# Performance work log

Measured on AMD Instinct MI355X. Metric: run time of the kernel, lower is better.

The kernel has to match this reference:

```python
import jax, jax.numpy as jnp
import numpy as np

B, S, D, M, NQ = 256, 200, 128, 64, 5000
A_TRI, B_TRI, C_TRI = 0.01, 0.05, 0.1  # triangular membership params a,b,c


def setup_inputs():
    key = jax.random.key(0)
    ks = jax.random.split(key, 16)
    g = lambda k, shp: jax.random.normal(k, shp, dtype=jnp.float32) * 0.05
    return dict(
        question_seq=jax.random.randint(ks[0], (B, S), 0, NQ),
        correctness_seq=jax.random.randint(ks[1], (B, S), 0, 2),
        Mk=g(ks[2], (M, D)),
        Mv0=g(ks[3], (M, D)),
        emb_concept=g(ks[4], (NQ, D)),
        emb_interaction=g(ks[5], (2 * NQ, D)),
        Wf=g(ks[6], (D, 2 * D)), bf=jnp.zeros((D,), jnp.float32),
        Wa=g(ks[7], (D, 2 * D)), ba=jnp.zeros((D,), jnp.float32),
        We=g(ks[8], (D, D)), be=jnp.zeros((D,), jnp.float32),
        Wadd=g(ks[9], (D, D)), badd=jnp.zeros((D,), jnp.float32),
        W_ih=g(ks[10], (4 * D, D)), W_hh=g(ks[11], (4 * D, D)),
        b_ih=jnp.zeros((4 * D,), jnp.float32), b_hh=jnp.zeros((4 * D,), jnp.float32),
        hx0=g(ks[12], (1, D)), cx0=g(ks[13], (1, D)),
        Wp=g(ks[14], (1, D)), bp=jnp.zeros((1,), jnp.float32),
    )


def _skvmn(Mk, Mv0, emb_concept, emb_interaction, Wf, bf, Wa, ba, We, be,
           Wadd, badd, W_ih, W_hh, b_ih, b_hh, hx0, cx0, Wp, bp,
           question_seq, correctness_seq):
    concept = emb_concept[question_seq]                                # [B,S,D]
    inter = emb_interaction[question_seq + NQ * correctness_seq]        # [B,S,D]

    # ---- DKVMN key addressing + value memory read/erase/add recurrence ----
    def mem_step(mem, xs):
        k_t, y_t = xs                                                   # [B,D]
        cw = jax.nn.softmax(k_t @ Mk.T, axis=1)                         # [B,M]
        read = jnp.einsum('bm,bmd->bd', cw, mem)                        # [B,D]
        f = jnp.tanh(jnp.concatenate([read, k_t], 1) @ Wf.T + bf)       # [B,D]
        we = jnp.concatenate([f, y_t], 1) @ Wa.T + ba                   # write embed
        erase = jax.nn.sigmoid(we @ We.T + be)
        add = jnp.tanh(we @ Wadd.T + badd)
        mem = mem * (1.0 - cw[:, :, None] * erase[:, None, :]) \
              + cw[:, :, None] * add[:, None, :]
        return mem, (cw, f)

    mem0 = jnp.broadcast_to(Mv0[None], (B, M, D)).astype(jnp.float32)
    _, (w, ft) = jax.lax.scan(
        mem_step, mem0,
        (concept.transpose(1, 0, 2), inter.transpose(1, 0, 2)))
    # w: [S,B,M], ft: [S,B,D]

    # ---- triangular layer: bin correlation weights into identity vectors ----
    wb = w.transpose(1, 0, 2)                                           # [B,S,M]
    tri = jnp.minimum((wb - A_TRI) / (B_TRI - A_TRI),
                      (C_TRI - wb) / (C_TRI - B_TRI))
    tri = jnp.maximum(tri, 0.0)
    iv = jnp.where(tri >= 0.6, 2.0, jnp.where(tri >= 0.1, 1.0, 0.0))    # [B,S,M]

    sq = jnp.sum(iv * iv, axis=2)                                       # [B,S]
    dist = sq[:, :, None] + sq[:, None, :] - 2.0 * jnp.einsum('btm,bjm->btj', iv, iv)
    NEG = jnp.float32(-1e32)
    d2 = jnp.where(dist > 0.0, NEG, dist)
    triu = jnp.triu(jnp.ones((S, S), bool), k=0)                        # mask j >= t
    d2 = jnp.where(triu[None], NEG, d2)
    idx_mat = jnp.arange(S * S, dtype=jnp.float32).reshape(S, S)
    score = d2 + idx_mat[None]                                          # [B,S,S]
    prev_t = jnp.argmax(score, axis=2)                                  # [B,S] prior matching step
    valid = jnp.max(score, axis=2) >= 0.0                               # [B,S]

    # ---- hop-LSTM: substitute hx with hidden state of prior matching step ----
    def lstm_step(carry, xs):
        hx, cx, H = carry
        t, x_t, prev_b, valid_b = xs
        h_prev = H[prev_b, jnp.arange(B)]                               # gather [B,D]
        hx = jnp.where(valid_b[:, None], h_prev, hx)
        gates = x_t @ W_ih.T + b_ih + hx @ W_hh.T + b_hh
        i_, f_, g_, o_ = jnp.split(gates, 4, axis=1)
        cx = jax.nn.sigmoid(f_) * cx + jax.nn.sigmoid(i_) * jnp.tanh(g_)
        hx = jax.nn.sigmoid(o_) * jnp.tanh(cx)
        H = jax.lax.dynamic_update_slice(H, hx[None], (t, 0, 0))
        return (hx, cx, H), hx

    H0 = jnp.zeros((S, B, D), jnp.float32)
    hx = jnp.broadcast_to(hx0, (B, D)).astype(jnp.float32)
    cx = jnp.broadcast_to(cx0, (B, D)).astype(jnp.float32)
    _, hs = jax.lax.scan(lstm_step, (hx, cx, H0),
                         (jnp.arange(S), ft, prev_t.T, valid.T))         # hs: [S,B,D]

    logits = jnp.einsum('sbd,d->sb', hs, Wp[0]) + bp[0]
    return jax.nn.sigmoid(logits).T                                     # [B,S]


def reference(question_seq, correctness_seq, Mk, Mv0, emb_concept, emb_interaction,
              Wf, bf, Wa, ba, We, be, Wadd, badd, W_ih, W_hh, b_ih, b_hh,
              hx0, cx0, Wp, bp):
    return _skvmn(Mk, Mv0, emb_concept, emb_interaction, Wf, bf, Wa, ba, We, be,
                  Wadd, badd, W_ih, W_hh, b_ih, b_hh, hx0, cx0, Wp, bp,
                  question_seq, correctness_seq)
```

## Files before the change

kernel.cpp:

```cpp
#include <hip/hip_runtime.h>

typedef unsigned int u32;
typedef unsigned short u16;
typedef unsigned long long u64;
typedef _Float16 f16;
typedef _Float16 f16x2 __attribute__((ext_vector_type(2)));

#define Bn 256
#define Sn 200
#define Dn 128
#define Mn 64
#define NQn 5000

__device__ __forceinline__ float fdot2f(u32 w, u32 x, float acc) {
#if __has_builtin(__builtin_amdgcn_fdot2)
    return __builtin_amdgcn_fdot2(__builtin_bit_cast(f16x2, w),
                                  __builtin_bit_cast(f16x2, x), acc, false);
#else
    f16x2 a = __builtin_bit_cast(f16x2, w);
    f16x2 b = __builtin_bit_cast(f16x2, x);
    return acc + (float)a[0] * (float)b[0] + (float)a[1] * (float)b[1];
#endif
}

__device__ __forceinline__ u32 packh2(float a, float b) {
    u16 ua = __builtin_bit_cast(u16, (f16)a);
    u16 ub = __builtin_bit_cast(u16, (f16)b);
    return (u32)ua | ((u32)ub << 16);
}

__device__ __forceinline__ float h2f(u16 u) { return (float)__builtin_bit_cast(f16, u); }
__device__ __forceinline__ float h2lo(u32 v) { return h2f((u16)(v & 0xffff)); }
__device__ __forceinline__ float h2hi(u32 v) { return h2f((u16)(v >> 16)); }

__device__ __forceinline__ float fexp2f(float x) {
#if __has_builtin(__builtin_amdgcn_exp2f)
    return __builtin_amdgcn_exp2f(x);
#else
    return exp2f(x);
#endif
}
__device__ __forceinline__ float frcpf(float x) {
#if __has_builtin(__builtin_amdgcn_rcpf)
    return __builtin_amdgcn_rcpf(x);
#else
    return 1.0f / x;
#endif
}
__device__ __forceinline__ float sig_fast(float x)  { return frcpf(1.0f + fexp2f(-1.44269504f * x)); }
__device__ __forceinline__ float tanh_fast(float x) { return fmaf(-2.0f, frcpf(1.0f + fexp2f(2.88539008f * x)), 1.0f); }

__global__ __launch_bounds__(512) void phase0_kernel(
    const int* __restrict__ qseq,
    const float* __restrict__ Mk, const float* __restrict__ embc,
    u16* __restrict__ cw16, ulonglong2* __restrict__ codes)
{
    __shared__ float MkT[Dn * 65];
    __shared__ float kb[8][Dn];
    int tid = threadIdx.x;
    for (int idx = tid; idx < Mn * Dn; idx += 512) {
        int m = idx >> 7, d = idx & 127;
        MkT[d * 65 + m] = Mk[idx];
    }
    __syncthreads();
    int w = tid >> 6, lane = tid & 63;
    int item = blockIdx.x * 8 + w;
    int qq = qseq[item];
    kb[w][lane]      = embc[qq * Dn + lane];
    kb[w][lane + 64] = embc[qq * Dn + lane + 64];
    __syncthreads();
    float acc = 0.0f;
    const float* kw = kb[w];
#pragma unroll 8
    for (int d = 0; d < Dn; ++d)
        acc = fmaf(MkT[d * 65 + lane], kw[d], acc);
    float mx = acc;
    for (int off = 32; off; off >>= 1) mx = fmaxf(mx, __shfl_xor(mx, off));
    float e = expf(acc - mx);
    float sm = e;
    for (int off = 32; off; off >>= 1) sm += __shfl_xor(sm, off);
    float cw = e / sm;
    cw16[item * Mn + lane] = __builtin_bit_cast(u16, (f16)cw);
    float t1 = (cw - 0.01f) / (0.05f - 0.01f);
    float t2 = (0.1f - cw) / (0.1f - 0.05f);
    float tri = fminf(t1, t2);
    tri = fmaxf(tri, 0.0f);
    int iv = (tri >= 0.6f) ? 2 : ((tri >= 0.1f) ? 1 : 0);
    u64 b1 = __ballot(iv >= 1);
    u64 b2 = __ballot(iv == 2);
    if (lane == 0) { codes[item].x = b1; codes[item].y = b2; }
}

__global__ __launch_bounds__(256) void match_kernel(
    const ulonglong2* __restrict__ codes, int* __restrict__ prev)
{
    __shared__ u64 clo[Sn], chi[Sn];
    int b = blockIdx.x, tid = threadIdx.x;
    if (tid < Sn) { ulonglong2 c = codes[b * Sn + tid]; clo[tid] = c.x; chi[tid] = c.y; }
    __syncthreads();
    if (tid < Sn) {
        u64 mylo = clo[tid], myhi = chi[tid];
        int best = -1;
        for (int j = 0; j < tid; ++j)
            if (clo[j] == mylo && chi[j] == myhi) best = j;
        prev[b * Sn + tid] = best;
    }
}

__global__ __launch_bounds__(512) void setup_kernel(
    const float* __restrict__ Wa, const float* __restrict__ We,
    const float* __restrict__ Wadd,
    const float* __restrict__ ba, const float* __restrict__ be,
    const float* __restrict__ badd,
    float* __restrict__ CEf, float* __restrict__ CAf,
    float* __restrict__ CEy, float* __restrict__ CAy,
    float* __restrict__ c0s)
{
    __shared__ float weR[128], waR[128];
    int d = blockIdx.x, tid = threadIdx.x;
    if (tid < 128) weR[tid] = We[d * 128 + tid];
    else if (tid < 256) waR[tid - 128] = Wadd[d * 128 + (tid - 128)];
    __syncthreads();
    int mat = tid >> 7, j = tid & 127;
    const float* src = (mat == 0 || mat == 2) ? weR : waR;
    int col = (mat < 2) ? j : (128 + j);
    float acc = 0.0f;
    for (int k = 0; k < 128; ++k) acc = fmaf(src[k], Wa[k * 256 + col], acc);
    float* dst = (mat == 0) ? CEf : (mat == 1) ? CAf : (mat == 2) ? CEy : CAy;
    dst[d * 128 + j] = acc;
    if (tid == 0) {
        float a = 0.0f;
        for (int k = 0; k < 128; ++k) a = fmaf(weR[k], ba[k], a);
        c0s[d] = a + be[d];
    } else if (tid == 1) {
        float a = 0.0f;
        for (int k = 0; k < 128; ++k) a = fmaf(waR[k], ba[k], a);
        c0s[128 + d] = a + badd[d];
    }
}

__global__ __launch_bounds__(512) void rowk_kernel(
    const float* __restrict__ W, const float* __restrict__ emb,
    u16* __restrict__ outp)
{
    __shared__ u32 wL[128 * 65];
    __shared__ u32 vb[8][64];
    int tid = threadIdx.x;
    for (int idx = tid; idx < 128 * 64; idx += 512) {
        int dd = idx >> 6, jj = idx & 63;
        const float2 wv = *(const float2*)(W + dd * 256 + 128 + 2 * jj);
        wL[dd * 65 + jj] = packh2(wv.x, wv.y);
    }
    int w = tid >> 6, lane = tid & 63;
    int row = blockIdx.x * 8 + w;
    {
        const float2 kv = *(const float2*)(emb + row * Dn + 2 * lane);
        vb[w][lane] = packh2(kv.x, kv.y);
    }
    __syncthreads();
    const u32* w0 = wL + lane * 65;
    const u32* w1 = wL + (64 + lane) * 65;
    const u32* x  = vb[w];
    float a0 = 0, a1 = 0, b0 = 0, b1 = 0;
#pragma unroll
    for (int jj = 0; jj < 64; jj += 2) {
        a0 = fdot2f(w0[jj],     x[jj],     a0);
        a1 = fdot2f(w0[jj + 1], x[jj + 1], a1);
        b0 = fdot2f(w1[jj],     x[jj],     b0);
        b1 = fdot2f(w1[jj + 1], x[jj + 1], b1);
    }
    outp[row * Dn + lane]      = __builtin_bit_cast(u16, (f16)(a0 + a1));
    outp[row * Dn + 64 + lane] = __builtin_bit_cast(u16, (f16)(b0 + b1));
}

__global__ __launch_bounds__(512) void rowe_kernel(
    const float* __restrict__ CEy, const float* __restrict__ CAy,
    const float* __restrict__ c0s, const float* __restrict__ embi,
    u16* __restrict__ ebR, u16* __restrict__ abR)
{
    __shared__ u32 eL[128 * 65];
    __shared__ u32 aL[128 * 65];
    __shared__ u32 vb[8][64];
    __shared__ float c0L[256];
    int tid = threadIdx.x;
    for (int idx = tid; idx < 128 * 64; idx += 512) {
        int dd = idx >> 6, jj = idx & 63;
        const float2 e2 = *(const float2*)(CEy + dd * 128 + 2 * jj);
        const float2 a2 = *(const float2*)(CAy + dd * 128 + 2 * jj);
        eL[dd * 65 + jj] = packh2(e2.x, e2.y);
        aL[dd * 65 + jj] = packh2(a2.x, a2.y);
    }
    if (tid < 256) c0L[tid] = c0s[tid];
    int w = tid >> 6, lane = tid & 63;
    int row = blockIdx.x * 8 + w;
    {
        const float2 kv = *(const float2*)(embi + row * Dn + 2 * lane);
        vb[w][lane] = packh2(kv.x, kv.y);
    }
    __syncthreads();
    const u32* x   = vb[w];
    const u32* e0p = eL + lane * 65;
    const u32* e1p = eL + (64 + lane) * 65;
    const u32* a0p = aL + lane * 65;
    const u32* a1p = aL + (64 + lane) * 65;
    float ea0 = 0, ea1 = 0, eb0 = 0, eb1 = 0;
    float aa0 = 0, aa1 = 0, ab0 = 0, ab1 = 0;
#pragma unroll
    for (int jj = 0; jj < 64; jj += 2) {
        ea0 = fdot2f(e0p[jj],     x[jj],     ea0);
        ea1 = fdot2f(e0p[jj + 1], x[jj + 1], ea1);
        eb0 = fdot2f(e1p[jj],     x[jj],     eb0);
        eb1 = fdot2f(e1p[jj + 1], x[jj + 1], eb1);
        aa0 = fdot2f(a0p[jj],     x[jj],     aa0);
        aa1 = fdot2f(a0p[jj + 1], x[jj + 1], aa1);
        ab0 = fdot2f(a1p[jj],     x[jj],     ab0);
        ab1 = fdot2f(a1p[jj + 1], x[jj + 1], ab1);
    }
    ebR[row * Dn + lane]      = __builtin_bit_cast(u16, (f16)(ea0 + ea1 + c0L[lane]));
    ebR[row * Dn + 64 + lane] = __builtin_bit_cast(u16, (f16)(eb0 + eb1 + c0L[64 + lane]));
    abR[row * Dn + lane]      = __builtin_bit_cast(u16, (f16)(aa0 + aa1 + c0L[128 + lane]));
    abR[row * Dn + 64 + lane] = __builtin_bit_cast(u16, (f16)(ab0 + ab1 + c0L[192 + lane]));
}

__global__ __launch_bounds__(512, 1) void fused_kernel(
    const float* __restrict__ Mv0,
    const float* __restrict__ Wf, const float* __restrict__ bfv,
    const float* __restrict__ CEf, const float* __restrict__ CAf,
    const u16* __restrict__ cw16, const u16* __restrict__ kfR,
    const u16* __restrict__ ebR, const u16* __restrict__ abR,
    const int* __restrict__ qseq, const int* __restrict__ cseq,
    const float* __restrict__ W_ih, const float* __restrict__ W_hh,
    const float* __restrict__ b_ih, const float* __restrict__ b_hh,
    const float* __restrict__ hx0, const float* __restrict__ cx0,
    const float* __restrict__ Wp, const float* __restrict__ bp,
    const int* __restrict__ prev,
    float* __restrict__ out)
{
    __shared__ u32 cwL[Sn * 32];
    __shared__ __align__(16) u32 kfb[2][16 * 64];
    __shared__ __align__(16) u32 ebb[2][16 * 64];
    __shared__ __align__(16) u32 abb[2][16 * 64];
    __shared__ __align__(16) u32 rbuf[64], fbuf[64];
    __shared__ __align__(16) u32 HL[(Sn + 1) * 64];
    __shared__ float bfL[Dn];
    __shared__ int qrowL[Sn], irowL[Sn], prevL[Sn];
    __shared__ u32 wpL[64];
    __shared__ float bpL;

    int tid = threadIdx.x;
    int d = tid >> 2, q = tid & 3;
    int b = blockIdx.x;

    u32 wfr[16], wew[16], wadw[16];
    {
        const float2* wf2 = (const float2*)(Wf  + d * 256 + q * 32);
        const float2* we2 = (const float2*)(CEf + d * 128 + q * 32);
        const float2* wd2 = (const float2*)(CAf + d * 128 + q * 32);
#pragma unroll
        for (int i = 0; i < 16; ++i) {
            float2 a;
            a = wf2[i]; wfr[i]  = packh2(a.x, a.y);
            a = we2[i]; wew[i]  = packh2(a.x, a.y);
            a = wd2[i]; wadw[i] = packh2(a.x, a.y);
        }
    }
    u32 wx[4][16], wh[4][16];
    float bias[4];
#pragma unroll
    for (int g = 0; g < 4; ++g) {
        const float2* wi2 = (const float2*)(W_ih + (size_t)(g * 128 + d) * Dn + q * 32);
        const float2* wh2 = (const float2*)(W_hh + (size_t)(g * 128 + d) * Dn + q * 32);
#pragma unroll
        for (int i = 0; i < 16; ++i) {
            float2 a;
            a = wi2[i]; wx[g][i] = packh2(a.x, a.y);
            a = wh2[i]; wh[g][i] = packh2(a.x, a.y);
        }
        bias[g] = b_ih[g * 128 + d] + b_hh[g * 128 + d];
    }
    float memv[16];
#pragma unroll
    for (int i = 0; i < 16; ++i) memv[i] = Mv0[(q * 16 + i) * Dn + d];
    float cx = cx0[d];

    if (tid < Dn) bfL[tid] = bfv[tid];
    if (tid < 64) {
        HL[tid]  = packh2(hx0[2 * tid], hx0[2 * tid + 1]);
        wpL[tid] = packh2(Wp[2 * tid], Wp[2 * tid + 1]);
    }
    if (tid == 0) bpL = bp[0];
    if (tid < Sn) {
        int qq = qseq[b * Sn + tid];
        qrowL[tid] = qq;
        irowL[tid] = qq + NQn * cseq[b * Sn + tid];
        prevL[tid] = prev[b * Sn + tid];
    }
    __syncthreads();

    for (int i = tid; i < Sn * 32; i += 512) cwL[i] = ((const u32*)cw16)[b * Sn * 32 + i];
    for (int i = tid; i < 1024; i += 512) {
        int s = i >> 6, off = i & 63;
        kfb[0][i] = ((const u32*)kfR)[qrowL[s] * 64 + off];
        ebb[0][i] = ((const u32*)ebR)[irowL[s] * 64 + off];
        abb[0][i] = ((const u32*)abR)[irowL[s] * 64 + off];
    }
    __syncthreads();

    u32 cwp[8];
#pragma unroll
    for (int i = 0; i < 8; ++i) cwp[i] = cwL[q * 8 + i];

    for (int t = 0; t < Sn; ++t) {
        int sl = (t >> 4) & 1, ti = t & 15;
        if (ti == 0) {
            int c1 = (t >> 4) + 1;
            if (c1 * 16 < Sn) {
                int n = (Sn - c1 * 16 < 16 ? Sn - c1 * 16 : 16) * 64;
                for (int i = tid; i < n; i += 512) {
                    int s = i >> 6, off = i & 63;
                    int t2 = c1 * 16 + s;
                    kfb[sl ^ 1][i] = ((const u32*)kfR)[qrowL[t2] * 64 + off];
                    ebb[sl ^ 1][i] = ((const u32*)ebR)[irowL[t2] * 64 + off];
                    abb[sl ^ 1][i] = ((const u32*)abR)[irowL[t2] * 64 + off];
                }
            }
        }
        float p0 = 0, p1 = 0, p2 = 0, p3 = 0;
#pragma unroll
        for (int i = 0; i < 4; ++i) {
            p0 = fmaf(h2lo(cwp[i]),     memv[2 * i],     p0);
            p1 = fmaf(h2hi(cwp[i]),     memv[2 * i + 1], p1);
            p2 = fmaf(h2lo(cwp[4 + i]), memv[8 + 2 * i], p2);
            p3 = fmaf(h2hi(cwp[4 + i]), memv[9 + 2 * i], p3);
        }
        float pr = (p0 + p1) + (p2 + p3);
        pr += __shfl_xor(pr, 1);
        pr += __shfl_xor(pr, 2);
        if (q == 0) ((f16*)rbuf)[d] = (f16)pr;
        __syncthreads();
        u16 kfc = ((const u16*)(kfb[sl]))[ti * 128 + d];
        u16 ebc = ((const u16*)(ebb[sl]))[ti * 128 + d];
        u16 abc = ((const u16*)(abb[sl]))[ti * 128 + d];
        float a0 = 0, a1 = 0, a2 = 0, a3 = 0;
#pragma unroll
        for (int u = 0; u < 4; ++u) {
            uint4 x = ((const uint4*)rbuf)[(q << 2) + u];
            a0 = fdot2f(wfr[4 * u + 0], x.x, a0);
            a1 = fdot2f(wfr[4 * u + 1], x.y, a1);
            a2 = fdot2f(wfr[4 * u + 2], x.z, a2);
            a3 = fdot2f(wfr[4 * u + 3], x.w, a3);
        }
        float accf = (a0 + a1) + (a2 + a3);
        accf += __shfl_xor(accf, 1);
        accf += __shfl_xor(accf, 2);
        float fv = tanh_fast(accf + h2f(kfc) + bfL[d]);
        if (q == 0) ((f16*)fbuf)[d] = (f16)fv;
        __syncthreads();
        int pv = prevL[t];
        int hrow = (pv >= 0) ? (pv + 1) : t;
        const uint4* h4 = (const uint4*)(HL + hrow * 64 + q * 16);
        float e0 = 0, e1 = 0, g0 = 0, g1 = 0;
        float s0 = 0, s1 = 0, s2 = 0, s3 = 0;
#pragma unroll
        for (int u = 0; u < 4; ++u) {
            uint4 x = ((const uint4*)fbuf)[(q << 2) + u];
            uint4 y = h4[u];
            e0 = fdot2f(wew[4 * u + 0], x.x, e0);   g0 = fdot2f(wadw[4 * u + 0], x.x, g0);
            e1 = fdot2f(wew[4 * u + 1], x.y, e1);   g1 = fdot2f(wadw[4 * u + 1], x.y, g1);
            e0 = fdot2f(wew[4 * u + 2], x.z, e0);   g0 = fdot2f(wadw[4 * u + 2], x.z, g0);
            e1 = fdot2f(wew[4 * u + 3], x.w, e1);   g1 = fdot2f(wadw[4 * u + 3], x.w, g1);
            s0 = fdot2f(wx[0][4 * u + 0], x.x, s0);
            s0 = fdot2f(wx[0][4 * u + 1], x.y, s0);
            s0 = fdot2f(wx[0][4 * u + 2], x.z, s0);
            s0 = fdot2f(wx[0][4 * u + 3], x.w, s0);
            s0 = fdot2f(wh[0][4 * u + 0], y.x, s0);
            s0 = fdot2f(wh[0][4 * u + 1], y.y, s0);
            s0 = fdot2f(wh[0][4 * u + 2], y.z, s0);
            s0 = fdot2f(wh[0][4 * u + 3], y.w, s0);
            s1 = fdot2f(wx[1][4 * u + 0], x.x, s1);
            s1 = fdot2f(wx[1][4 * u + 1], x.y, s1);
            s1 = fdot2f(wx[1][4 * u + 2], x.z, s1);
            s1 = fdot2f(wx[1][4 * u + 3], x.w, s1);
            s1 = fdot2f(wh[1][4 * u + 0], y.x, s1);
            s1 = fdot2f(wh[1][4 * u + 1], y.y, s1);
            s1 = fdot2f(wh[1][4 * u + 2], y.z, s1);
            s1 = fdot2f(wh[1][4 * u + 3], y.w, s1);
            s2 = fdot2f(wx[2][4 * u + 0], x.x, s2);
            s2 = fdot2f(wx[2][4 * u + 1], x.y, s2);
            s2 = fdot2f(wx[2][4 * u + 2], x.z, s2);
            s2 = fdot2f(wx[2][4 * u + 3], x.w, s2);
            s2 = fdot2f(wh[2][4 * u + 0], y.x, s2);
            s2 = fdot2f(wh[2][4 * u + 1], y.y, s2);
            s2 = fdot2f(wh[2][4 * u + 2], y.z, s2);
            s2 = fdot2f(wh[2][4 * u + 3], y.w, s2);
            s3 = fdot2f(wx[3][4 * u + 0], x.x, s3);
            s3 = fdot2f(wx[3][4 * u + 1], x.y, s3);
            s3 = fdot2f(wx[3][4 * u + 2], x.z, s3);
            s3 = fdot2f(wx[3][4 * u + 3], x.w, s3);
            s3 = fdot2f(wh[3][4 * u + 0], y.x, s3);
            s3 = fdot2f(wh[3][4 * u + 1], y.y, s3);
            s3 = fdot2f(wh[3][4 * u + 2], y.z, s3);
            s3 = fdot2f(wh[3][4 * u + 3], y.w, s3);
        }
        float pe = e0 + e1, pa = g0 + g1;
        pe += __shfl_xor(pe, 1); pe += __shfl_xor(pe, 2);
        pa += __shfl_xor(pa, 1); pa += __shfl_xor(pa, 2);
        float ev = sig_fast(pe + h2f(ebc));
        float av = tanh_fast(pa + h2f(abc));
        s0 += __shfl_xor(s0, 1); s0 += __shfl_xor(s0, 2);
        s1 += __shfl_xor(s1, 1); s1 += __shfl_xor(s1, 2);
        s2 += __shfl_xor(s2, 1); s2 += __shfl_xor(s2, 2);
        s3 += __shfl_xor(s3, 1); s3 += __shfl_xor(s3, 2);
        float ig  = sig_fast(s0 + bias[0]);
        float fgt = sig_fast(s1 + bias[1]);
        float gg  = tanh_fast(s2 + bias[2]);
        float og  = sig_fast(s3 + bias[3]);
        cx = fmaf(fgt, cx, ig * gg);
        float hv = og * tanh_fast(cx);
        if (q == 0) ((f16*)HL)[(t + 1) * Dn + d] = (f16)hv;
        u32 cwn[8];
        if (t + 1 < Sn) {
#pragma unroll
            for (int i = 0; i < 8; ++i) cwn[i] = cwL[(t + 1) * 32 + q * 8 + i];
        }
#pragma unroll
        for (int i = 0; i < 8; ++i) {
            float lo = h2lo(cwp[i]), hi = h2hi(cwp[i]);
            float t0 = fmaf(-ev, memv[2 * i],     av);
            float t1 = fmaf(-ev, memv[2 * i + 1], av);
            memv[2 * i]     = fmaf(lo, t0, memv[2 * i]);
            memv[2 * i + 1] = fmaf(hi, t1, memv[2 * i + 1]);
        }
        if (t + 1 < Sn) {
#pragma unroll
            for (int i = 0; i < 8; ++i) cwp[i] = cwn[i];
        }
    }
    __syncthreads();
    if (tid < Sn) {
        float acc = 0.0f;
        const u32* hr = HL + (tid + 1) * 64;
#pragma unroll 8
        for (int j = 0; j < 64; ++j) {
            int jj = (j + tid) & 63;
            acc = fdot2f(hr[jj], wpL[jj], acc);
        }
        out[b * Sn + tid] = sig_fast(acc + bpL);
    }
}

extern "C" void kernel_launch(void* const* d_in, const int* in_sizes, int n_in,
                              void* d_out, int out_size, void* d_ws, size_t ws_size,
                              hipStream_t stream) {
    const int*   qseq = (const int*)d_in[0];
    const int*   cseq = (const int*)d_in[1];
    const float* Mk   = (const float*)d_in[2];
    const float* Mv0  = (const float*)d_in[3];
    const float* embc = (const float*)d_in[4];
    const float* embi = (const float*)d_in[5];
    const float* Wf   = (const float*)d_in[6];
    const float* bfv  = (const float*)d_in[7];
    const float* Wa   = (const float*)d_in[8];
    const float* bav  = (const float*)d_in[9];
    const float* We   = (const float*)d_in[10];
    const float* bev  = (const float*)d_in[11];
    const float* Wadd = (const float*)d_in[12];
    const float* badv = (const float*)d_in[13];
    const float* W_ih = (const float*)d_in[14];
    const float* W_hh = (const float*)d_in[15];
    const float* b_ih = (const float*)d_in[16];
    const float* b_hh = (const float*)d_in[17];
    const float* hx0  = (const float*)d_in[18];
    const float* cx0  = (const float*)d_in[19];
    const float* Wp   = (const float*)d_in[20];
    const float* bp   = (const float*)d_in[21];
    float* out = (float*)d_out;

    char* ws = (char*)d_ws;
    u16* cw16 = (u16*)ws;
    ulonglong2* codes = (ulonglong2*)(ws + 6553600);
    int* prev = (int*)(ws + 7372800);
    u16* kfR  = (u16*)(ws + 7577600);
    u16* ebR  = (u16*)(ws + 8857600);
    u16* abR  = (u16*)(ws + 11417600);
    float* CEf = (float*)(ws + 13977600);
    float* CAf = (float*)(ws + 14043136);
    float* CEy = (float*)(ws + 14108672);
    float* CAy = (float*)(ws + 14174208);
    float* c0s = (float*)(ws + 14239744);

    setup_kernel<<<128, 512, 0, stream>>>(Wa, We, Wadd, bav, bev, badv,
                                          CEf, CAf, CEy, CAy, c0s);
    phase0_kernel<<<(Bn * Sn) / 8, 512, 0, stream>>>(qseq, Mk, embc, cw16, codes);
    rowk_kernel<<<NQn / 8, 512, 0, stream>>>(Wf, embc, kfR);
    rowe_kernel<<<(2 * NQn) / 8, 512, 0, stream>>>(CEy, CAy, c0s, embi, ebR, abR);
    match_kernel<<<Bn, 256, 0, stream>>>(codes, prev);
    fused_kernel<<<Bn, 512, 0, stream>>>(Mv0, Wf, bfv, CEf, CAf,
                                         cw16, kfR, ebR, abR, qseq, cseq,
                                         W_ih, W_hh, b_ih, b_hh, hx0, cx0, Wp, bp,
                                         prev, out);
}
```

Before: 709.0 us.

## Split each feature row across eight threads in fused recurrence kernel

Doubles the fused kernel's block to 1024 threads so each hidden dimension is handled by 8 lanes instead of 4. This halves the per-thread register weights, memory slice and dot-product lengths, at the cost of an extra shuffle-reduction stage per dot product. The LSTM gate biases move from registers to shared memory, and the next-step address-weight prefetch is replaced by a direct shared-memory load each step. The aim is to shorten the serial per-timestep critical path with more parallel lanes. The risks are higher sync cost with 16 waves per block and added register pressure under the 1024-thread limit.

```diff
diff --git a/kernel.cpp b/kernel.cpp
--- a/kernel.cpp
+++ b/kernel.cpp
@@ -222,7 +222,7 @@
     abR[row * Dn + 64 + lane] = __builtin_bit_cast(u16, (f16)(ab0 + ab1 + c0L[192 + lane]));
 }
 
-__global__ __launch_bounds__(512, 1) void fused_kernel(
+__global__ __launch_bounds__(1024) void fused_kernel(
     const float* __restrict__ Mv0,
     const float* __restrict__ Wf, const float* __restrict__ bfv,
     const float* __restrict__ CEf, const float* __restrict__ CAf,
@@ -243,47 +243,47 @@
     __shared__ __align__(16) u32 rbuf[64], fbuf[64];
     __shared__ __align__(16) u32 HL[(Sn + 1) * 64];
     __shared__ float bfL[Dn];
+    __shared__ float biasL[512];
     __shared__ int qrowL[Sn], irowL[Sn], prevL[Sn];
     __shared__ u32 wpL[64];
     __shared__ float bpL;
 
     int tid = threadIdx.x;
-    int d = tid >> 2, q = tid & 3;
+    int d = tid >> 3, q = tid & 7;
     int b = blockIdx.x;
 
-    u32 wfr[16], wew[16], wadw[16];
+    u32 wfr[8], wew[8], wadw[8];
     {
-        const float2* wf2 = (const float2*)(Wf  + d * 256 + q * 32);
-        const float2* we2 = (const float2*)(CEf + d * 128 + q * 32);
-        const float2* wd2 = (const float2*)(CAf + d * 128 + q * 32);
-#pragma unroll
-        for (int i = 0; i < 16; ++i) {
+        const float2* wf2 = (const float2*)(Wf  + d * 256 + q * 16);
+        const float2* we2 = (const float2*)(CEf + d * 128 + q * 16);
+        const float2* wd2 = (const float2*)(CAf + d * 128 + q * 16);
+#pragma unroll
+        for (int i = 0; i < 8; ++i) {
             float2 a;
             a = wf2[i]; wfr[i]  = packh2(a.x, a.y);
             a = we2[i]; wew[i]  = packh2(a.x, a.y);
             a = wd2[i]; wadw[i] = packh2(a.x, a.y);
         }
     }
-    u32 wx[4][16], wh[4][16];
-    float bias[4];
+    u32 wx[4][8], wh[4][8];
 #pragma unroll
     for (int g = 0; g < 4; ++g) {
-        const float2* wi2 = (const float2*)(W_ih + (size_t)(g * 128 + d) * Dn + q * 32);
-        const float2* wh2 = (const float2*)(W_hh + (size_t)(g * 128 + d) * Dn + q * 32);
-#pragma unroll
-        for (int i = 0; i < 16; ++i) {
+        const float2* wi2 = (const float2*)(W_ih + (size_t)(g * 128 + d) * Dn + q * 16);
+        const float2* wh2 = (const float2*)(W_hh + (size_t)(g * 128 + d) * Dn + q * 16);
+#pragma unroll
+        for (int i = 0; i < 8; ++i) {
             float2 a;
             a = wi2[i]; wx[g][i] = packh2(a.x, a.y);
             a = wh2[i]; wh[g][i] = packh2(a.x, a.y);
         }
-        bias[g] = b_ih[g * 128 + d] + b_hh[g * 128 + d];
-    }
-    float memv[16];
-#pragma unroll
-    for (int i = 0; i < 16; ++i) memv[i] = Mv0[(q * 16 + i) * Dn + d];
+    }
+    float memv[8];
+#pragma unroll
+    for (int i = 0; i < 8; ++i) memv[i] = Mv0[(q * 8 + i) * Dn + d];
     float cx = cx0[d];
 
     if (tid < Dn) bfL[tid] = bfv[tid];
+    if (tid < 512) biasL[tid] = b_ih[tid] + b_hh[tid];
     if (tid < 64) {
         HL[tid]  = packh2(hx0[2 * tid], hx0[2 * tid + 1]);
         wpL[tid] = packh2(Wp[2 * tid], Wp[2 * tid + 1]);
@@ -297,18 +297,14 @@
     }
     __syncthreads();
 
-    for (int i = tid; i < Sn * 32; i += 512) cwL[i] = ((const u32*)cw16)[b * Sn * 32 + i];
-    for (int i = tid; i < 1024; i += 512) {
+    for (int i = tid; i < Sn * 32; i += 1024) cwL[i] = ((const u32*)cw16)[b * Sn * 32 + i];
+    for (int i = tid; i < 1024; i += 1024) {
         int s = i >> 6, off = i & 63;
         kfb[0][i] = ((const u32*)kfR)[qrowL[s] * 64 + off];
         ebb[0][i] = ((const u32*)ebR)[irowL[s] * 64 + off];
         abb[0][i] = ((const u32*)abR)[irowL[s] * 64 + off];
     }
     __syncthreads();
-
-    u32 cwp[8];
-#pragma unroll
-    for (int i = 0; i < 8; ++i) cwp[i] = cwL[q * 8 + i];
 
     for (int t = 0; t < Sn; ++t) {
         int sl = (t >> 4) & 1, ti = t & 15;
@@ -316,7 +312,7 @@
             int c1 = (t >> 4) + 1;
             if (c1 * 16 < Sn) {
                 int n = (Sn - c1 * 16 < 16 ? Sn - c1 * 16 : 16) * 64;
-                for (int i = tid; i < n; i += 512) {
+                for (int i = tid; i < n; i += 1024) {
                     int s = i >> 6, off = i & 63;
                     int t2 = c1 * 16 + s;
                     kfb[sl ^ 1][i] = ((const u32*)kfR)[qrowL[t2] * 64 + off];
@@ -325,17 +321,21 @@
                 }
             }
         }
+        u32 cwp[4];
+#pragma unroll
+        for (int i = 0; i < 4; ++i) cwp[i] = cwL[t * 32 + q * 4 + i];
         float p0 = 0, p1 = 0, p2 = 0, p3 = 0;
 #pragma unroll
-        for (int i = 0; i < 4; ++i) {
+        for (int i = 0; i < 2; ++i) {
             p0 = fmaf(h2lo(cwp[i]),     memv[2 * i],     p0);
             p1 = fmaf(h2hi(cwp[i]),     memv[2 * i + 1], p1);
-            p2 = fmaf(h2lo(cwp[4 + i]), memv[8 + 2 * i], p2);
-            p3 = fmaf(h2hi(cwp[4 + i]), memv[9 + 2 * i], p3);
+            p2 = fmaf(h2lo(cwp[2 + i]), memv[4 + 2 * i], p2);
+            p3 = fmaf(h2hi(cwp[2 + i]), memv[5 + 2 * i], p3);
         }
         float pr = (p0 + p1) + (p2 + p3);
         pr += __shfl_xor(pr, 1);
         pr += __shfl_xor(pr, 2);
+        pr += __shfl_xor(pr, 4);
         if (q == 0) ((f16*)rbuf)[d] = (f16)pr;
         __syncthreads();
         u16 kfc = ((const u16*)(kfb[sl]))[ti * 128 + d];
@@ -343,8 +343,8 @@
         u16 abc = ((const u16*)(abb[sl]))[ti * 128 + d];
         float a0 = 0, a1 = 0, a2 = 0, a3 = 0;
 #pragma unroll
-        for (int u = 0; u < 4; ++u) {
-            uint4 x = ((const uint4*)rbuf)[(q << 2) + u];
+        for (int u = 0; u < 2; ++u) {
+            uint4 x = ((const uint4*)rbuf)[(q << 1) + u];
             a0 = fdot2f(wfr[4 * u + 0], x.x, a0);
             a1 = fdot2f(wfr[4 * u + 1], x.y, a1);
             a2 = fdot2f(wfr[4 * u + 2], x.z, a2);
@@ -353,22 +353,24 @@
         float accf = (a0 + a1) + (a2 + a3);
         accf += __shfl_xor(accf, 1);
         accf += __shfl_xor(accf, 2);
+        accf += __shfl_xor(accf, 4);
         float fv = tanh_fast(accf + h2f(kfc) + bfL[d]);
         if (q == 0) ((f16*)fbuf)[d] = (f16)fv;
         __syncthreads();
         int pv = prevL[t];
         int hrow = (pv >= 0) ? (pv + 1) : t;
-        const uint4* h4 = (const uint4*)(HL + hrow * 64 + q * 16);
-        float e0 = 0, e1 = 0, g0 = 0, g1 = 0;
+        const uint4* h4 = (const uint4*)(HL + hrow * 64) + (q << 1);
+        const uint4* f4 = (const uint4*)fbuf + (q << 1);
+        float ec = 0, gc = 0;
         float s0 = 0, s1 = 0, s2 = 0, s3 = 0;
 #pragma unroll
-        for (int u = 0; u < 4; ++u) {
-            uint4 x = ((const uint4*)fbuf)[(q << 2) + u];
+        for (int u = 0; u < 2; ++u) {
+            uint4 x = f4[u];
             uint4 y = h4[u];
-            e0 = fdot2f(wew[4 * u + 0], x.x, e0);   g0 = fdot2f(wadw[4 * u + 0], x.x, g0);
-            e1 = fdot2f(wew[4 * u + 1], x.y, e1);   g1 = fdot2f(wadw[4 * u + 1], x.y, g1);
-            e0 = fdot2f(wew[4 * u + 2], x.z, e0);   g0 = fdot2f(wadw[4 * u + 2], x.z, g0);
-            e1 = fdot2f(wew[4 * u + 3], x.w, e1);   g1 = fdot2f(wadw[4 * u + 3], x.w, g1);
+            ec = fdot2f(wew[4 * u + 0], x.x, ec);   gc = fdot2f(wadw[4 * u + 0], x.x, gc);
+            ec = fdot2f(wew[4 * u + 1], x.y, ec);   gc = fdot2f(wadw[4 * u + 1], x.y, gc);
+            ec = fdot2f(wew[4 * u + 2], x.z, ec);   gc = fdot2f(wadw[4 * u + 2], x.z, gc);
+            ec = fdot2f(wew[4 * u + 3], x.w, ec);   gc = fdot2f(wadw[4 * u + 3], x.w, gc);
             s0 = fdot2f(wx[0][4 * u + 0], x.x, s0);
             s0 = fdot2f(wx[0][4 * u + 1], x.y, s0);
             s0 = fdot2f(wx[0][4 * u + 2], x.z, s0);
@@ -402,38 +404,28 @@
             s3 = fdot2f(wh[3][4 * u + 2], y.z, s3);
             s3 = fdot2f(wh[3][4 * u + 3], y.w, s3);
         }
-        float pe = e0 + e1, pa = g0 + g1;
-        pe += __shfl_xor(pe, 1); pe += __shfl_xor(pe, 2);
-        pa += __shfl_xor(pa, 1); pa += __shfl_xor(pa, 2);
-        float ev = sig_fast(pe + h2f(ebc));
-        float av = tanh_fast(pa + h2f(abc));
-        s0 += __shfl_xor(s0, 1); s0 += __shfl_xor(s0, 2);
-        s1 += __shfl_xor(s1, 1); s1 += __shfl_xor(s1, 2);
-        s2 += __shfl_xor(s2, 1); s2 += __shfl_xor(s2, 2);
-        s3 += __shfl_xor(s3, 1); s3 += __shfl_xor(s3, 2);
-        float ig  = sig_fast(s0 + bias[0]);
-        float fgt = sig_fast(s1 + bias[1]);
-        float gg  = tanh_fast(s2 + bias[2]);
-        float og  = sig_fast(s3 + bias[3]);
+        ec += __shfl_xor(ec, 1); ec += __shfl_xor(ec, 2); ec += __shfl_xor(ec, 4);
+        gc += __shfl_xor(gc, 1); gc += __shfl_xor(gc, 2); gc += __shfl_xor(gc, 4);
+        float ev = sig_fast(ec + h2f(ebc));
+        float av = tanh_fast(gc + h2f(abc));
+        s0 += __shfl_xor(s0, 1); s0 += __shfl_xor(s0, 2); s0 += __shfl_xor(s0, 4);
+        s1 += __shfl_xor(s1, 1); s1 += __shfl_xor(s1, 2); s1 += __shfl_xor(s1, 4);
+        s2 += __shfl_xor(s2, 1); s2 += __shfl_xor(s2, 2); s2 += __shfl_xor(s2, 4);
+        s3 += __shfl_xor(s3, 1); s3 += __shfl_xor(s3, 2); s3 += __shfl_xor(s3, 4);
+        float ig  = sig_fast(s0 + biasL[d]);
+        float fgt = sig_fast(s1 + biasL[128 + d]);
+        float gg  = tanh_fast(s2 + biasL[256 + d]);
+        float og  = sig_fast(s3 + biasL[384 + d]);
         cx = fmaf(fgt, cx, ig * gg);
         float hv = og * tanh_fast(cx);
         if (q == 0) ((f16*)HL)[(t + 1) * Dn + d] = (f16)hv;
-        u32 cwn[8];
-        if (t + 1 < Sn) {
-#pragma unroll
-            for (int i = 0; i < 8; ++i) cwn[i] = cwL[(t + 1) * 32 + q * 8 + i];
-        }
-#pragma unroll
-        for (int i = 0; i < 8; ++i) {
+#pragma unroll
+        for (int i = 0; i < 4; ++i) {
             float lo = h2lo(cwp[i]), hi = h2hi(cwp[i]);
             float t0 = fmaf(-ev, memv[2 * i],     av);
             float t1 = fmaf(-ev, memv[2 * i + 1], av);
             memv[2 * i]     = fmaf(lo, t0, memv[2 * i]);
             memv[2 * i + 1] = fmaf(hi, t1, memv[2 * i + 1]);
-        }
-        if (t + 1 < Sn) {
-#pragma unroll
-            for (int i = 0; i < 8; ++i) cwp[i] = cwn[i];
         }
     }
     __syncthreads();
@@ -495,8 +487,8 @@
     rowk_kernel<<<NQn / 8, 512, 0, stream>>>(Wf, embc, kfR);
     rowe_kernel<<<(2 * NQn) / 8, 512, 0, stream>>>(CEy, CAy, c0s, embi, ebR, abR);
     match_kernel<<<Bn, 256, 0, stream>>>(codes, prev);
-    fused_kernel<<<Bn, 512, 0, stream>>>(Mv0, Wf, bfv, CEf, CAf,
-                                         cw16, kfR, ebR, abR, qseq, cseq,
-                                         W_ih, W_hh, b_ih, b_hh, hx0, cx0, Wp, bp,
-                                         prev, out);
-}
+    fused_kernel<<<Bn, 1024, 0, stream>>>(Mv0, Wf, bfv, CEf, CAf,
+                                          cw16, kfR, ebR, abR, qseq, cseq,
+                                          W_ih, W_hh, b_ih, b_hh, hx0, cx0, Wp, bp,
+                                          prev, out);
+}
```

Result: slower. 850.3 us (+19.9%).
